# Kernel tuning notes

Hardware: AMD Instinct MI355X
Metric: run time of the kernel (lower is better)

## Reference

```python
import jax, jax.numpy as jnp
import numpy as np
from jax import lax

N_NEURONS = 128
BATCH = 2048
SEQ = 128
INFTY = 1e8


def setup_inputs() -> dict:
    key = jax.random.key(0)
    ks = jax.random.split(key, 10)
    n = N_NEURONS
    lim = 1.0 / np.sqrt(n)  # torch LSTMCell default init scale
    return {
        "enc_outputs": jax.random.normal(ks[0], (BATCH, SEQ, n), jnp.float32),
        "h0": jax.random.normal(ks[1], (BATCH, n), jnp.float32),
        "c0": jax.random.normal(ks[2], (BATCH, n), jnp.float32),
        "dec_first_input": jnp.zeros((1, n), jnp.float32),
        "W_ref": jax.random.normal(ks[3], (1, n, n), jnp.float32),
        "W_out": jax.random.normal(ks[4], (n, n), jnp.float32),
        "v": jax.random.normal(ks[5], (n,), jnp.float32),
        "W_ih": jax.random.uniform(ks[6], (4 * n, n), jnp.float32, -lim, lim),
        "W_hh": jax.random.uniform(ks[7], (4 * n, n), jnp.float32, -lim, lim),
        "b_ih": jax.random.uniform(ks[8], (4 * n,), jnp.float32, -lim, lim),
        "b_hh": jax.random.uniform(ks[9], (4 * n,), jnp.float32, -lim, lim),
    }


def _decode(enc_outputs, h0, c0, dec_first_input, W_ref, W_out, v, W_ih, W_hh, b_ih, b_hh):
    B, S, n = enc_outputs.shape
    # step-invariant pointer projection of encoder outputs (the conv1d term)
    enc_term = jnp.einsum("bsn,mn->bsm", enc_outputs, W_ref[0])  # [B,S,n]
    batch_idx = jnp.arange(B)
    keys = jax.random.split(jax.random.key(1234), S)
    inp0 = jnp.broadcast_to(dec_first_input, (B, n))
    mask0 = jnp.zeros((B, S), enc_outputs.dtype)

    def step(carry, key):
        h, c, mask, inp = carry
        # LSTMCell: gate order i, f, g, o (torch convention)
        gates = inp @ W_ih.T + b_ih + h @ W_hh.T + b_hh  # [B,4n]
        i_g, f_g, g_g, o_g = jnp.split(gates, 4, axis=1)
        c = jax.nn.sigmoid(f_g) * c + jax.nn.sigmoid(i_g) * jnp.tanh(g_g)
        h = jax.nn.sigmoid(o_g) * jnp.tanh(c)
        # pointer attention scores
        dec_term = (h @ W_out)[:, None, :]  # [B,1,n]
        scores = jnp.sum(v * jnp.tanh(enc_term + dec_term), axis=-1)  # [B,S]
        masked = scores - INFTY * mask
        loc = jax.random.categorical(key, masked)  # [B] int, non-differentiable sample
        logp = jnp.take_along_axis(jax.nn.log_softmax(masked, axis=1), loc[:, None], axis=1)[:, 0]
        mask = mask.at[batch_idx, loc].set(1.0)
        inp = enc_outputs[batch_idx, loc, :]  # gather next decoder input
        return (h, c, mask, inp), (loc, logp)

    _, (locs, logps) = lax.scan(step, (h0, c0, mask0, inp0), keys)
    locs = locs.T  # [B,S]
    tour = jnp.concatenate([locs, locs[:, :1]], axis=1)  # append first location
    log_prob = jnp.sum(logps, axis=0)  # [B]
    return log_prob, tour


def reference(enc_outputs, h0, c0, dec_first_input, W_ref, W_out, v, W_ih, W_hh, b_ih, b_hh):
    return _decode(enc_outputs, h0, c0, dec_first_input, W_ref, W_out, v, W_ih, W_hh, b_ih, b_hh)
```

## Files before the change

kernel.cpp:

```cpp
#include <hip/hip_runtime.h>
#include <cstdint>
#include <cstddef>

#pragma clang fp contract(off)

#define PRNG_PARTITIONABLE 1

#define INFTY_F 1.0e8f
#define TINY_F 1.17549435e-38f

__device__ __forceinline__ float fdiv_rn(float n, float q) {
  float y0 = __builtin_amdgcn_rcpf(q);
  float y  = fmaf(fmaf(-q, y0, 1.0f), y0, y0);
  float r0 = n * y;
  float e0 = fmaf(-q, r0, n);
  float r1 = fmaf(e0, y, r0);
  float e1 = fmaf(-q, r1, n);
  return fmaf(e1, y, r1);
}

__device__ __forceinline__ void tf2x32(uint32_t k0, uint32_t k1, uint32_t x0, uint32_t x1,
                                       uint32_t& o0, uint32_t& o1) {
  uint32_t ks2 = k0 ^ k1 ^ 0x1BD11BDAu;
  uint32_t v0 = x0 + k0, v1 = x1 + k1;
#define TF_R(r) { v0 += v1; v1 = (v1 << (r)) | (v1 >> (32 - (r))); v1 ^= v0; }
  TF_R(13) TF_R(15) TF_R(26) TF_R(6)
  v0 += k1;  v1 += ks2 + 1u;
  TF_R(17) TF_R(29) TF_R(16) TF_R(24)
  v0 += ks2; v1 += k0 + 2u;
  TF_R(13) TF_R(15) TF_R(26) TF_R(6)
  v0 += k0;  v1 += k1 + 3u;
  TF_R(17) TF_R(29) TF_R(16) TF_R(24)
  v0 += k1;  v1 += ks2 + 4u;
  TF_R(13) TF_R(15) TF_R(26) TF_R(6)
  v0 += ks2; v1 += k0 + 5u;
#undef TF_R
  o0 = v0; o1 = v1;
}

__device__ __forceinline__ uint32_t random_bits32(uint32_t k0, uint32_t k1, uint32_t j) {
#if PRNG_PARTITIONABLE
  uint32_t o0, o1;
  tf2x32(k0, k1, 0u, j, o0, o1);
  return o0 ^ o1;
#else
  uint32_t o0, o1;
  if (j < 131072u) { tf2x32(k0, k1, j, j + 131072u, o0, o1); return o0; }
  else             { tf2x32(k0, k1, j - 131072u, j, o0, o1); return o1; }
#endif
}

__device__ __forceinline__ float xla_tanhf(float x) {
  float xc = fminf(fmaxf(x, -9.0f), 9.0f);
  float x2 = xc * xc;
  float p = -2.76076847742355e-16f;
  p = (p * x2) + 2.00018790482477e-13f;
  p = (p * x2) + -8.60467152213735e-11f;
  p = (p * x2) + 5.12229709037114e-08f;
  p = (p * x2) + 1.48572235717979e-05f;
  p = (p * x2) + 6.37261928875436e-04f;
  p = (p * x2) + 4.89352455891786e-03f;
  float num = xc * p;
  float q = 1.19825839466702e-06f;
  q = (q * x2) + 1.18534705686654e-04f;
  q = (q * x2) + 2.26843463243900e-03f;
  q = (q * x2) + 4.89352518554385e-03f;
  float r = num / q;
  return (fabsf(x) < 0.0004f) ? x : r;
}

__device__ __forceinline__ void xla_tanh2(float xa, float xb, float& ra, float& rb) {
  float xca = fminf(fmaxf(xa, -9.0f), 9.0f);
  float xcb = fminf(fmaxf(xb, -9.0f), 9.0f);
  float x2a = xca * xca, x2b = xcb * xcb;
  float pa = -2.76076847742355e-16f, pb = -2.76076847742355e-16f;
  pa = (pa * x2a) + 2.00018790482477e-13f;  pb = (pb * x2b) + 2.00018790482477e-13f;
  pa = (pa * x2a) + -8.60467152213735e-11f; pb = (pb * x2b) + -8.60467152213735e-11f;
  pa = (pa * x2a) + 5.12229709037114e-08f;  pb = (pb * x2b) + 5.12229709037114e-08f;
  pa = (pa * x2a) + 1.48572235717979e-05f;  pb = (pb * x2b) + 1.48572235717979e-05f;
  pa = (pa * x2a) + 6.37261928875436e-04f;  pb = (pb * x2b) + 6.37261928875436e-04f;
  pa = (pa * x2a) + 4.89352455891786e-03f;  pb = (pb * x2b) + 4.89352455891786e-03f;
  float na = xca * pa, nb = xcb * pb;
  float qa = 1.19825839466702e-06f, qb = 1.19825839466702e-06f;
  qa = (qa * x2a) + 1.18534705686654e-04f; qb = (qb * x2b) + 1.18534705686654e-04f;
  qa = (qa * x2a) + 2.26843463243900e-03f; qb = (qb * x2b) + 2.26843463243900e-03f;
  qa = (qa * x2a) + 4.89352518554385e-03f; qb = (qb * x2b) + 4.89352518554385e-03f;
  float da = fdiv_rn(na, qa), db = fdiv_rn(nb, qb);
  ra = (fabsf(xa) < 0.0004f) ? xa : da;
  rb = (fabsf(xb) < 0.0004f) ? xb : db;
}

__device__ __forceinline__ float xla_expf(float x) {
  x = fminf(x, 88.3762626647950f);
  x = fmaxf(x, -88.3762626647949f);
  float m = floorf((x * 1.44269504088896341f) + 0.5f);
  float r = x - (m * 0.693359375f);
  r = r - (m * -2.12194440e-4f);
  float r2 = r * r;
  float y = 1.9875691500E-4f;
  y = (y * r) + 1.3981999507E-3f;
  y = (y * r) + 8.3334519073E-3f;
  y = (y * r) + 4.1665795894E-2f;
  y = (y * r) + 1.6666665459E-1f;
  y = (y * r) + 5.0000001201E-1f;
  y = (y * r2) + r;
  y = y + 1.0f;
  int mi = (int)m;
  float s = __uint_as_float((uint32_t)((mi + 127) << 23));
  return y * s;
}

__device__ __forceinline__ float xla_sigmoidf(float x) {
  return 1.0f / (1.0f + xla_expf(-x));
}

__device__ __forceinline__ float xla_logf(float x) {
  uint32_t b = __float_as_uint(x);
  float e = (float)((int)(b >> 23) - 126);
  float m = __uint_as_float((b & 0x007fffffu) | 0x3f000000u);
  bool mlt = (m < 0.707106781186547524f);
  float tmp = mlt ? m : 0.0f;
  e = e - (mlt ? 1.0f : 0.0f);
  float xx = (m - 1.0f) + tmp;
  float z = xx * xx;
  float y = 7.0376836292E-2f;
  y = (y * xx) + -1.1514610310E-1f;
  y = (y * xx) + 1.1676998740E-1f;
  y = (y * xx) + -1.2420140846E-1f;
  y = (y * xx) + 1.4249322787E-1f;
  y = (y * xx) + -1.6668057665E-1f;
  y = (y * xx) + 2.0000714765E-1f;
  y = (y * xx) + -2.4999993993E-1f;
  y = (y * xx) + 3.3333331174E-1f;
  y = y * xx;
  y = y * z;
  y = y + (e * -2.12194440e-4f);
  y = y - (z * 0.5f);
  float res = xx + y;
  res = res + (e * 0.693359375f);
  return res;
}

__device__ __forceinline__ float gumbel_from_bits(uint32_t bits) {
  float f = __uint_as_float((bits >> 9) | 0x3f800000u) - 1.0f;
  float u = (f * 1.0f) + TINY_F;
  u = fmaxf(TINY_F, u);
  return -xla_logf(-xla_logf(u));
}

__global__ void k_keys(uint32_t* __restrict__ keys) {
  int t = threadIdx.x;
  if (t >= 128) return;
#if PRNG_PARTITIONABLE
  uint32_t o0, o1;
  tf2x32(0u, 1234u, 0u, (uint32_t)t, o0, o1);
  keys[2 * t] = o0; keys[2 * t + 1] = o1;
#else
  uint32_t o0, o1, a, bb;
  if (t < 64) {
    tf2x32(0u, 1234u, (uint32_t)(2 * t),     (uint32_t)(128 + 2 * t), o0, o1); a  = o0;
    tf2x32(0u, 1234u, (uint32_t)(2 * t + 1), (uint32_t)(129 + 2 * t), o0, o1); bb = o0;
  } else {
    tf2x32(0u, 1234u, (uint32_t)(2 * t - 128), (uint32_t)(2 * t),     o0, o1); a  = o1;
    tf2x32(0u, 1234u, (uint32_t)(2 * t - 127), (uint32_t)(2 * t + 1), o0, o1); bb = o1;
  }
  keys[2 * t] = a; keys[2 * t + 1] = bb;
#endif
}

__global__ void k_trans(const float* __restrict__ Wih, const float* __restrict__ Whh,
                        float* __restrict__ WihT, float* __restrict__ WhhT) {
  int idx = blockIdx.x * blockDim.x + threadIdx.x;
  if (idx < 65536) {
    int r = idx >> 7, k = idx & 127;
    WihT[k * 512 + r] = Wih[idx];
    WhhT[k * 512 + r] = Whh[idx];
  }
}

__global__ __launch_bounds__(128) void k_encT(const float* __restrict__ enc,
                                              const float* __restrict__ Wref,
                                              float* __restrict__ encT) {
  __shared__ float el[64 * 132];
  __shared__ float ot[64 * 129];
  int tid = threadIdx.x;
  int b  = blockIdx.x >> 1;
  int sh = blockIdx.x & 1;
  const float* eb = enc + (size_t)b * 16384 + (size_t)sh * 8192;
  for (int i = tid; i < 8192; i += 128) {
    int s = i >> 7, n = i & 127;
    el[s * 132 + n] = eb[i];
  }
  __syncthreads();
  int sl = tid & 63;
  int mh = tid >> 6;
  for (int ml = 0; ml < 64; ++ml) {
    int m = mh * 64 + ml;
    const float4* wr = (const float4*)(Wref + m * 128);
    float acc = 0.0f;
#pragma unroll 8
    for (int q = 0; q < 32; ++q) {
      float4 w4 = wr[q];
      float4 e4 = *(const float4*)&el[sl * 132 + 4 * q];
      acc = fmaf(e4.x, w4.x, acc); acc = fmaf(e4.y, w4.y, acc);
      acc = fmaf(e4.z, w4.z, acc); acc = fmaf(e4.w, w4.w, acc);
    }
    ot[sl * 129 + m] = acc;
  }
  __syncthreads();
  float* op = encT + (size_t)b * 16384 + (size_t)(sh * 64) * 128;
  for (int i = tid; i < 8192; i += 128)
    op[i] = ot[(i >> 7) * 129 + (i & 127)];
}

__global__ __launch_bounds__(512) void k_encIH(const float* __restrict__ enc,
                                               const float* __restrict__ WihT,
                                               float* __restrict__ encIH) {
  __shared__ float el[32][128];
  const int r = threadIdx.x;
  const int b = blockIdx.x >> 2;
  const int q = blockIdx.x & 3;
  const float* eb = enc + (size_t)b * 16384 + (size_t)q * 4096;
  for (int i = r; i < 4096; i += 512)
    el[i >> 7][i & 127] = eb[i];
  __syncthreads();
  float acc[32];
#pragma unroll
  for (int s = 0; s < 32; ++s) acc[s] = 0.0f;
  const float* wp = WihT + r;
  for (int kc = 0; kc < 8; ++kc) {
    float wv[16];
#pragma unroll
    for (int j = 0; j < 16; ++j) wv[j] = wp[(size_t)(kc * 16 + j) * 512];
#pragma unroll
    for (int s = 0; s < 32; ++s) {
#pragma unroll
      for (int j = 0; j < 16; ++j)
        acc[s] = fmaf(el[s][kc * 16 + j], wv[j], acc[s]);
    }
  }
  float* op = encIH + ((size_t)b * 128 + (size_t)q * 32) * 512 + r;
#pragma unroll
  for (int s = 0; s < 32; ++s)
    op[(size_t)s * 512] = acc[s];
}

template <bool PRE>
__global__ __launch_bounds__(512, 4) void k_main(
    const float* __restrict__ enc, const float* __restrict__ h0,
    const float* __restrict__ c0, const float* __restrict__ dec_first,
    const float* __restrict__ W_out, const float* __restrict__ v,
    const float* __restrict__ b_ih, const float* __restrict__ b_hh,
    const float* __restrict__ WihT, const float* __restrict__ WhhT,
    const float* __restrict__ encT, const float* __restrict__ encIH,
    const uint32_t* __restrict__ keys, float* __restrict__ out) {
  __shared__ float xI_s[128][8];
  __shared__ float c_s[4][128];
  __shared__ float gates_s[4][512];
  __shared__ float2 vdec2_s[4][128];
  __shared__ float bih_s[512];
  __shared__ float bhh_s[512];
  __shared__ float v_s[128];
  __shared__ uint32_t keys_s[256];
  __shared__ int cu_s[4][128];
  __shared__ int pos_s[4][128];
  __shared__ int locs_s[4];
  __shared__ float red_va[4][2];
  __shared__ int   red_ia[4][2];
  __shared__ float red_mx[4][2];
  __shared__ float red_se[4][2];
  __shared__ float red_msel[4];

  const int tid  = threadIdx.x;
  const int lane = tid & 63;
  const int w    = tid >> 6;
  const int g4   = w >> 1;
  const int half = w & 1;
  const int s4   = half * 64 + lane;
  const int bbase = blockIdx.x * 4;
  const int b4   = bbase + g4;

  bih_s[tid] = b_ih[tid];
  bhh_s[tid] = b_hh[tid];
  if (tid < 256) keys_s[tid] = keys[tid];
  if (tid < 128) v_s[tid] = v[tid];
  {
    int g = tid >> 7, j = tid & 127;
    xI_s[j][g]     = dec_first[j];
    xI_s[j][4 + g] = h0[(size_t)(bbase + g) * 128 + j];
    c_s[g][j] = c0[(size_t)(bbase + g) * 128 + j];
    cu_s[g][j] = j;
    pos_s[g][j] = j;
  }
  float logp_sum = 0.0f;
  float* tour = out + 2048;
  __syncthreads();

  for (int step = 0; step < 128; ++step) {
    {
      const int r = tid;
      float aA0, aA1, aA2, aA3;
      float aB0 = 0.0f, aB1 = 0.0f, aB2 = 0.0f, aB3 = 0.0f;
      const float* phh = WhhT + r;
      if (PRE) {
        if (step == 0) {
          aA0 = aA1 = aA2 = aA3 = 0.0f;
        } else {
          aA0 = encIH[((size_t)(bbase + 0) * 128 + locs_s[0]) * 512 + r];
          aA1 = encIH[((size_t)(bbase + 1) * 128 + locs_s[1]) * 512 + r];
          aA2 = encIH[((size_t)(bbase + 2) * 128 + locs_s[2]) * 512 + r];
          aA3 = encIH[((size_t)(bbase + 3) * 128 + locs_s[3]) * 512 + r];
        }
#pragma unroll 4
        for (int k = 0; k < 128; ++k) {
          float4 xh = *(const float4*)&xI_s[k][4];
          float whh = phh[k * 512];
          aB0 = fmaf(xh.x, whh, aB0);
          aB1 = fmaf(xh.y, whh, aB1);
          aB2 = fmaf(xh.z, whh, aB2);
          aB3 = fmaf(xh.w, whh, aB3);
        }
      } else {
        aA0 = aA1 = aA2 = aA3 = 0.0f;
        const float* pih = WihT + r;
#pragma unroll 4
        for (int k = 0; k < 128; ++k) {
          float4 xi = *(const float4*)&xI_s[k][0];
          float4 xh = *(const float4*)&xI_s[k][4];
          float wih = pih[k * 512], whh = phh[k * 512];
          aA0 = fmaf(xi.x, wih, aA0);
          aA1 = fmaf(xi.y, wih, aA1);
          aA2 = fmaf(xi.z, wih, aA2);
          aA3 = fmaf(xi.w, wih, aA3);
          aB0 = fmaf(xh.x, whh, aB0);
          aB1 = fmaf(xh.y, whh, aB1);
          aB2 = fmaf(xh.z, whh, aB2);
          aB3 = fmaf(xh.w, whh, aB3);
        }
      }
      float b1 = bih_s[r], b2 = bhh_s[r];
      gates_s[0][r] = (((aA0 + b1) + aB0) + b2);
      gates_s[1][r] = (((aA1 + b1) + aB1) + b2);
      gates_s[2][r] = (((aA2 + b1) + aB2) + b2);
      gates_s[3][r] = (((aA3 + b1) + aB3) + b2);
    }
    __syncthreads();

    {
      int g = tid >> 7, j = tid & 127;
      float gi = gates_s[g][j], gf = gates_s[g][128 + j];
      float gg = gates_s[g][256 + j], go = gates_s[g][384 + j];
      float si = xla_sigmoidf(gi), sf = xla_sigmoidf(gf), so = xla_sigmoidf(go);
      float gt = xla_tanhf(gg);
      float cold = c_s[g][j];
      float cn = (sf * cold) + (si * gt);
      c_s[g][j] = cn;
      xI_s[j][4 + g] = so * xla_tanhf(cn);
    }
    __syncthreads();

    {
      int g = tid >> 7, m = tid & 127;
      float acc = 0.0f;
      const float* wo = W_out + m;
#pragma unroll 4
      for (int k = 0; k < 128; ++k)
        acc = fmaf(xI_s[k][4 + g], wo[k * 128], acc);
      vdec2_s[g][m] = make_float2(v_s[m], acc);
    }
    __syncthreads();

    const int u = 128 - step;
    const bool active = (s4 < u);
    float masked = -INFTY_F;
    float val = -INFTY_F;
    int   ia = 0x7fffffff;
    int   sc = 0;
    if (active) {
      sc = cu_s[g4][s4];
      const float* ep = encT + ((size_t)b4 * 128 + (size_t)sc) * 128;
      float acc = 0.0f;
#pragma unroll 4
      for (int m4 = 0; m4 < 32; ++m4) {
        float4 e4 = *(const float4*)&ep[4 * m4];
        float4 vd01 = *(const float4*)&vdec2_s[g4][4 * m4];
        float4 vd23 = *(const float4*)&vdec2_s[g4][4 * m4 + 2];
        float t0, t1, t2, t3;
        xla_tanh2(e4.x + vd01.y, e4.y + vd01.w, t0, t1);
        xla_tanh2(e4.z + vd23.y, e4.w + vd23.w, t2, t3);
        acc = acc + (vd01.x * t0);
        acc = acc + (vd01.z * t1);
        acc = acc + (vd23.x * t2);
        acc = acc + (vd23.z * t3);
      }
      masked = acc;
      uint32_t kk0 = keys_s[2 * step], kk1 = keys_s[2 * step + 1];
      uint32_t j0 = (uint32_t)b4 * 128u + (uint32_t)sc;
      float gmb = gumbel_from_bits(random_bits32(kk0, kk1, j0));
      val = gmb + masked;
      ia = sc;
    }
    {
      float va = val;
      float mx = masked;
#pragma unroll
      for (int off = 32; off > 0; off >>= 1) {
        float vo = __shfl_xor(va, off, 64);
        int io = __shfl_xor(ia, off, 64);
        if (vo > va || (vo == va && io < ia)) { va = vo; ia = io; }
        mx = fmaxf(mx, __shfl_xor(mx, off, 64));
      }
      float se = expf(masked - mx);
#pragma unroll
      for (int off = 32; off > 0; off >>= 1) se = se + __shfl_xor(se, off, 64);
      if (lane == 0) {
        red_va[g4][half] = va; red_ia[g4][half] = ia;
        red_mx[g4][half] = mx; red_se[g4][half] = se;
      }
      ia = active ? sc : 0x7fffffff;
    }
    __syncthreads();

    float mx2, lse2;
    {
      float vaA = red_va[g4][0], vaB = red_va[g4][1];
      int iaA = red_ia[g4][0], iaB = red_ia[g4][1];
      int loc = (vaB > vaA || (vaB == vaA && iaB < iaA)) ? iaB : iaA;
      if (active && sc == loc) {
        red_msel[g4] = masked;
        locs_s[g4] = loc;
        tour[(size_t)b4 * 129 + step] = (float)loc;
        if (step == 0) tour[(size_t)b4 * 129 + 128] = (float)loc;
        int p = pos_s[g4][loc];
        int last = cu_s[g4][u - 1];
        cu_s[g4][p] = last;
        pos_s[g4][last] = p;
      }
      const float* er = enc + (size_t)b4 * 16384 + (size_t)loc * 128;
      xI_s[s4][g4] = er[s4];
      float mxA = red_mx[g4][0], mxB = red_mx[g4][1];
      float seA = red_se[g4][0], seB = red_se[g4][1];
      mx2 = fmaxf(mxA, mxB);
      float se2 = seA * expf(mxA - mx2) + seB * expf(mxB - mx2);
      lse2 = logf(se2);
    }
    __syncthreads();
    logp_sum = logp_sum + ((red_msel[g4] - mx2) - lse2);
  }

  if (half == 0 && lane == 0) out[b4] = logp_sum;
}

extern "C" void kernel_launch(void* const* d_in, const int* in_sizes, int n_in,
                              void* d_out, int out_size, void* d_ws, size_t ws_size,
                              hipStream_t stream) {
  (void)in_sizes; (void)n_in; (void)out_size;
  const float* enc       = (const float*)d_in[0];
  const float* h0        = (const float*)d_in[1];
  const float* c0        = (const float*)d_in[2];
  const float* dec_first = (const float*)d_in[3];
  const float* W_ref     = (const float*)d_in[4];
  const float* W_out     = (const float*)d_in[5];
  const float* v         = (const float*)d_in[6];
  const float* W_ih      = (const float*)d_in[7];
  const float* W_hh      = (const float*)d_in[8];
  const float* b_ih      = (const float*)d_in[9];
  const float* b_hh      = (const float*)d_in[10];

  const size_t encT_elems  = (size_t)2048 * 16384;
  const size_t encIH_elems = (size_t)2048 * 128 * 512;
  size_t need_base = (encT_elems + 65536 + 65536) * sizeof(float) + 256 * sizeof(uint32_t);
  size_t need_pre  = need_base + encIH_elems * sizeof(float);
  if (ws_size < need_base) return;
  const bool pre = (ws_size >= need_pre);

  float* encT = (float*)d_ws;
  float* WihT = encT + encT_elems;
  float* WhhT = WihT + 65536;
  uint32_t* keys = (uint32_t*)(WhhT + 65536);
  float* encIH = (float*)(keys + 256);
  float* out = (float*)d_out;

  k_keys<<<dim3(1), dim3(128), 0, stream>>>(keys);
  k_trans<<<dim3(256), dim3(256), 0, stream>>>(W_ih, W_hh, WihT, WhhT);
  k_encT<<<dim3(4096), dim3(128), 0, stream>>>(enc, W_ref, encT);
  if (pre) {
    k_encIH<<<dim3(8192), dim3(512), 0, stream>>>(enc, WihT, encIH);
    k_main<true><<<dim3(512), dim3(512), 0, stream>>>(enc, h0, c0, dec_first, W_out, v,
                                                      b_ih, b_hh, WihT, WhhT, encT, encIH,
                                                      keys, out);
  } else {
    k_main<false><<<dim3(512), dim3(512), 0, stream>>>(enc, h0, c0, dec_first, W_out, v,
                                                       b_ih, b_hh, WihT, WhhT, encT, encIH,
                                                       keys, out);
  }
}
```

Baseline: 6.501 ms.

## Drop precomputed encoder-input gates and halve batch rows per block

Removes the k_encIH precompute pass and its large workspace buffer, so the input-to-hidden product is recomputed inside the step loop from WihT. Each block now handles 2 batch rows instead of 4 and the grid doubles to 1024 blocks, with launch bounds raised to 8 blocks per CU. The aim is more parallelism across the GPU and no large precompute write/read. The cost is that each step redoes the Wih matvec, and half the waves sit idle in the pointer phase while still joining the barriers.

```diff
diff --git a/kernel.cpp b/kernel.cpp
--- a/kernel.cpp
+++ b/kernel.cpp
@@ -213,81 +213,48 @@
     op[i] = ot[(i >> 7) * 129 + (i & 127)];
 }
 
-__global__ __launch_bounds__(512) void k_encIH(const float* __restrict__ enc,
-                                               const float* __restrict__ WihT,
-                                               float* __restrict__ encIH) {
-  __shared__ float el[32][128];
-  const int r = threadIdx.x;
-  const int b = blockIdx.x >> 2;
-  const int q = blockIdx.x & 3;
-  const float* eb = enc + (size_t)b * 16384 + (size_t)q * 4096;
-  for (int i = r; i < 4096; i += 512)
-    el[i >> 7][i & 127] = eb[i];
-  __syncthreads();
-  float acc[32];
-#pragma unroll
-  for (int s = 0; s < 32; ++s) acc[s] = 0.0f;
-  const float* wp = WihT + r;
-  for (int kc = 0; kc < 8; ++kc) {
-    float wv[16];
-#pragma unroll
-    for (int j = 0; j < 16; ++j) wv[j] = wp[(size_t)(kc * 16 + j) * 512];
-#pragma unroll
-    for (int s = 0; s < 32; ++s) {
-#pragma unroll
-      for (int j = 0; j < 16; ++j)
-        acc[s] = fmaf(el[s][kc * 16 + j], wv[j], acc[s]);
-    }
-  }
-  float* op = encIH + ((size_t)b * 128 + (size_t)q * 32) * 512 + r;
-#pragma unroll
-  for (int s = 0; s < 32; ++s)
-    op[(size_t)s * 512] = acc[s];
-}
-
-template <bool PRE>
-__global__ __launch_bounds__(512, 4) void k_main(
+__global__ __launch_bounds__(512, 8) void k_main(
     const float* __restrict__ enc, const float* __restrict__ h0,
     const float* __restrict__ c0, const float* __restrict__ dec_first,
     const float* __restrict__ W_out, const float* __restrict__ v,
     const float* __restrict__ b_ih, const float* __restrict__ b_hh,
     const float* __restrict__ WihT, const float* __restrict__ WhhT,
-    const float* __restrict__ encT, const float* __restrict__ encIH,
-    const uint32_t* __restrict__ keys, float* __restrict__ out) {
-  __shared__ float xI_s[128][8];
-  __shared__ float c_s[4][128];
-  __shared__ float gates_s[4][512];
-  __shared__ float2 vdec2_s[4][128];
+    const float* __restrict__ encT, const uint32_t* __restrict__ keys,
+    float* __restrict__ out) {
+  __shared__ float xI_s[128][4];
+  __shared__ float c_s[2][128];
+  __shared__ float gates_s[2][512];
+  __shared__ float2 vdec2_s[2][128];
   __shared__ float bih_s[512];
   __shared__ float bhh_s[512];
   __shared__ float v_s[128];
   __shared__ uint32_t keys_s[256];
-  __shared__ int cu_s[4][128];
-  __shared__ int pos_s[4][128];
-  __shared__ int locs_s[4];
-  __shared__ float red_va[4][2];
-  __shared__ int   red_ia[4][2];
-  __shared__ float red_mx[4][2];
-  __shared__ float red_se[4][2];
-  __shared__ float red_msel[4];
+  __shared__ int cu_s[2][128];
+  __shared__ int pos_s[2][128];
+  __shared__ float red_va[2][2];
+  __shared__ int   red_ia[2][2];
+  __shared__ float red_mx[2][2];
+  __shared__ float red_se[2][2];
+  __shared__ float red_msel[2];
 
   const int tid  = threadIdx.x;
   const int lane = tid & 63;
   const int w    = tid >> 6;
+  const bool pwave = (w < 4);
   const int g4   = w >> 1;
   const int half = w & 1;
   const int s4   = half * 64 + lane;
-  const int bbase = blockIdx.x * 4;
-  const int b4   = bbase + g4;
+  const int bbase = blockIdx.x * 2;
+  const int b4   = bbase + (pwave ? g4 : 0);
 
   bih_s[tid] = b_ih[tid];
   bhh_s[tid] = b_hh[tid];
   if (tid < 256) keys_s[tid] = keys[tid];
-  if (tid < 128) v_s[tid] = v[tid];
-  {
+  if (tid >= 256 && tid < 384) v_s[tid - 256] = v[tid - 256];
+  if (tid < 256) {
     int g = tid >> 7, j = tid & 127;
     xI_s[j][g]     = dec_first[j];
-    xI_s[j][4 + g] = h0[(size_t)(bbase + g) * 128 + j];
+    xI_s[j][2 + g] = h0[(size_t)(bbase + g) * 128 + j];
     c_s[g][j] = c0[(size_t)(bbase + g) * 128 + j];
     cu_s[g][j] = j;
     pos_s[g][j] = j;
@@ -299,54 +266,26 @@
   for (int step = 0; step < 128; ++step) {
     {
       const int r = tid;
-      float aA0, aA1, aA2, aA3;
-      float aB0 = 0.0f, aB1 = 0.0f, aB2 = 0.0f, aB3 = 0.0f;
+      float aA0 = 0.0f, aA1 = 0.0f, aB0 = 0.0f, aB1 = 0.0f;
+      const float* pih = WihT + r;
       const float* phh = WhhT + r;
-      if (PRE) {
-        if (step == 0) {
-          aA0 = aA1 = aA2 = aA3 = 0.0f;
-        } else {
-          aA0 = encIH[((size_t)(bbase + 0) * 128 + locs_s[0]) * 512 + r];
-          aA1 = encIH[((size_t)(bbase + 1) * 128 + locs_s[1]) * 512 + r];
-          aA2 = encIH[((size_t)(bbase + 2) * 128 + locs_s[2]) * 512 + r];
-          aA3 = encIH[((size_t)(bbase + 3) * 128 + locs_s[3]) * 512 + r];
-        }
 #pragma unroll 4
-        for (int k = 0; k < 128; ++k) {
-          float4 xh = *(const float4*)&xI_s[k][4];
-          float whh = phh[k * 512];
-          aB0 = fmaf(xh.x, whh, aB0);
-          aB1 = fmaf(xh.y, whh, aB1);
-          aB2 = fmaf(xh.z, whh, aB2);
-          aB3 = fmaf(xh.w, whh, aB3);
-        }
-      } else {
-        aA0 = aA1 = aA2 = aA3 = 0.0f;
-        const float* pih = WihT + r;
-#pragma unroll 4
-        for (int k = 0; k < 128; ++k) {
-          float4 xi = *(const float4*)&xI_s[k][0];
-          float4 xh = *(const float4*)&xI_s[k][4];
-          float wih = pih[k * 512], whh = phh[k * 512];
-          aA0 = fmaf(xi.x, wih, aA0);
-          aA1 = fmaf(xi.y, wih, aA1);
-          aA2 = fmaf(xi.z, wih, aA2);
-          aA3 = fmaf(xi.w, wih, aA3);
-          aB0 = fmaf(xh.x, whh, aB0);
-          aB1 = fmaf(xh.y, whh, aB1);
-          aB2 = fmaf(xh.z, whh, aB2);
-          aB3 = fmaf(xh.w, whh, aB3);
-        }
+      for (int k = 0; k < 128; ++k) {
+        float2 xi = *(const float2*)&xI_s[k][0];
+        float2 xh = *(const float2*)&xI_s[k][2];
+        float wih = pih[k * 512], whh = phh[k * 512];
+        aA0 = fmaf(xi.x, wih, aA0);
+        aA1 = fmaf(xi.y, wih, aA1);
+        aB0 = fmaf(xh.x, whh, aB0);
+        aB1 = fmaf(xh.y, whh, aB1);
       }
       float b1 = bih_s[r], b2 = bhh_s[r];
       gates_s[0][r] = (((aA0 + b1) + aB0) + b2);
       gates_s[1][r] = (((aA1 + b1) + aB1) + b2);
-      gates_s[2][r] = (((aA2 + b1) + aB2) + b2);
-      gates_s[3][r] = (((aA3 + b1) + aB3) + b2);
     }
     __syncthreads();
 
-    {
+    if (tid < 256) {
       int g = tid >> 7, j = tid & 127;
       float gi = gates_s[g][j], gf = gates_s[g][128 + j];
       float gg = gates_s[g][256 + j], go = gates_s[g][384 + j];
@@ -355,52 +294,52 @@
       float cold = c_s[g][j];
       float cn = (sf * cold) + (si * gt);
       c_s[g][j] = cn;
-      xI_s[j][4 + g] = so * xla_tanhf(cn);
+      xI_s[j][2 + g] = so * xla_tanhf(cn);
     }
     __syncthreads();
 
-    {
+    if (tid < 256) {
       int g = tid >> 7, m = tid & 127;
       float acc = 0.0f;
       const float* wo = W_out + m;
 #pragma unroll 4
       for (int k = 0; k < 128; ++k)
-        acc = fmaf(xI_s[k][4 + g], wo[k * 128], acc);
+        acc = fmaf(xI_s[k][2 + g], wo[k * 128], acc);
       vdec2_s[g][m] = make_float2(v_s[m], acc);
     }
     __syncthreads();
 
     const int u = 128 - step;
-    const bool active = (s4 < u);
-    float masked = -INFTY_F;
-    float val = -INFTY_F;
-    int   ia = 0x7fffffff;
-    int   sc = 0;
-    if (active) {
-      sc = cu_s[g4][s4];
-      const float* ep = encT + ((size_t)b4 * 128 + (size_t)sc) * 128;
-      float acc = 0.0f;
+    if (pwave) {
+      const bool active = (s4 < u);
+      float masked = -INFTY_F;
+      float val = -INFTY_F;
+      int   ia = 0x7fffffff;
+      int   sc = 0;
+      if (active) {
+        sc = cu_s[g4][s4];
+        const float* ep = encT + ((size_t)b4 * 128 + (size_t)sc) * 128;
+        float acc = 0.0f;
 #pragma unroll 4
-      for (int m4 = 0; m4 < 32; ++m4) {
-        float4 e4 = *(const float4*)&ep[4 * m4];
-        float4 vd01 = *(const float4*)&vdec2_s[g4][4 * m4];
-        float4 vd23 = *(const float4*)&vdec2_s[g4][4 * m4 + 2];
-        float t0, t1, t2, t3;
-        xla_tanh2(e4.x + vd01.y, e4.y + vd01.w, t0, t1);
-        xla_tanh2(e4.z + vd23.y, e4.w + vd23.w, t2, t3);
-        acc = acc + (vd01.x * t0);
-        acc = acc + (vd01.z * t1);
-        acc = acc + (vd23.x * t2);
-        acc = acc + (vd23.z * t3);
+        for (int m4 = 0; m4 < 32; ++m4) {
+          float4 e4 = *(const float4*)&ep[4 * m4];
+          float4 vd01 = *(const float4*)&vdec2_s[g4][4 * m4];
+          float4 vd23 = *(const float4*)&vdec2_s[g4][4 * m4 + 2];
+          float t0, t1, t2, t3;
+          xla_tanh2(e4.x + vd01.y, e4.y + vd01.w, t0, t1);
+          xla_tanh2(e4.z + vd23.y, e4.w + vd23.w, t2, t3);
+          acc = acc + (vd01.x * t0);
+          acc = acc + (vd01.z * t1);
+          acc = acc + (vd23.x * t2);
+          acc = acc + (vd23.z * t3);
+        }
+        masked = acc;
+        uint32_t kk0 = keys_s[2 * step], kk1 = keys_s[2 * step + 1];
+        uint32_t j0 = (uint32_t)b4 * 128u + (uint32_t)sc;
+        float gmb = gumbel_from_bits(random_bits32(kk0, kk1, j0));
+        val = gmb + masked;
+        ia = sc;
       }
-      masked = acc;
-      uint32_t kk0 = keys_s[2 * step], kk1 = keys_s[2 * step + 1];
-      uint32_t j0 = (uint32_t)b4 * 128u + (uint32_t)sc;
-      float gmb = gumbel_from_bits(random_bits32(kk0, kk1, j0));
-      val = gmb + masked;
-      ia = sc;
-    }
-    {
       float va = val;
       float mx = masked;
 #pragma unroll
@@ -417,38 +356,38 @@
         red_va[g4][half] = va; red_ia[g4][half] = ia;
         red_mx[g4][half] = mx; red_se[g4][half] = se;
       }
-      ia = active ? sc : 0x7fffffff;
+      __syncthreads();
+
+      {
+        float vaA = red_va[g4][0], vaB = red_va[g4][1];
+        int iaA = red_ia[g4][0], iaB = red_ia[g4][1];
+        int loc = (vaB > vaA || (vaB == vaA && iaB < iaA)) ? iaB : iaA;
+        if (active && sc == loc) {
+          red_msel[g4] = masked;
+          tour[(size_t)b4 * 129 + step] = (float)loc;
+          if (step == 0) tour[(size_t)b4 * 129 + 128] = (float)loc;
+          int p = pos_s[g4][loc];
+          int last = cu_s[g4][u - 1];
+          cu_s[g4][p] = last;
+          pos_s[g4][last] = p;
+        }
+        const float* er = enc + (size_t)b4 * 16384 + (size_t)loc * 128;
+        xI_s[s4][g4] = er[s4];
+        float mxA = red_mx[g4][0], mxB = red_mx[g4][1];
+        float seA = red_se[g4][0], seB = red_se[g4][1];
+        float mx2 = fmaxf(mxA, mxB);
+        float se2 = seA * expf(mxA - mx2) + seB * expf(mxB - mx2);
+        float lse2 = logf(se2);
+        __syncthreads();
+        logp_sum = logp_sum + ((red_msel[g4] - mx2) - lse2);
+      }
+    } else {
+      __syncthreads();
+      __syncthreads();
     }
-    __syncthreads();
-
-    float mx2, lse2;
-    {
-      float vaA = red_va[g4][0], vaB = red_va[g4][1];
-      int iaA = red_ia[g4][0], iaB = red_ia[g4][1];
-      int loc = (vaB > vaA || (vaB == vaA && iaB < iaA)) ? iaB : iaA;
-      if (active && sc == loc) {
-        red_msel[g4] = masked;
-        locs_s[g4] = loc;
-        tour[(size_t)b4 * 129 + step] = (float)loc;
-        if (step == 0) tour[(size_t)b4 * 129 + 128] = (float)loc;
-        int p = pos_s[g4][loc];
-        int last = cu_s[g4][u - 1];
-        cu_s[g4][p] = last;
-        pos_s[g4][last] = p;
-      }
-      const float* er = enc + (size_t)b4 * 16384 + (size_t)loc * 128;
-      xI_s[s4][g4] = er[s4];
-      float mxA = red_mx[g4][0], mxB = red_mx[g4][1];
-      float seA = red_se[g4][0], seB = red_se[g4][1];
-      mx2 = fmaxf(mxA, mxB);
-      float se2 = seA * expf(mxA - mx2) + seB * expf(mxB - mx2);
-      lse2 = logf(se2);
-    }
-    __syncthreads();
-    logp_sum = logp_sum + ((red_msel[g4] - mx2) - lse2);
-  }
-
-  if (half == 0 && lane == 0) out[b4] = logp_sum;
+  }
+
+  if (pwave && half == 0 && lane == 0) out[b4] = logp_sum;
 }
 
 extern "C" void kernel_launch(void* const* d_in, const int* in_sizes, int n_in,
@@ -467,31 +406,19 @@
   const float* b_ih      = (const float*)d_in[9];
   const float* b_hh      = (const float*)d_in[10];
 
-  const size_t encT_elems  = (size_t)2048 * 16384;
-  const size_t encIH_elems = (size_t)2048 * 128 * 512;
-  size_t need_base = (encT_elems + 65536 + 65536) * sizeof(float) + 256 * sizeof(uint32_t);
-  size_t need_pre  = need_base + encIH_elems * sizeof(float);
-  if (ws_size < need_base) return;
-  const bool pre = (ws_size >= need_pre);
+  const size_t encT_elems = (size_t)2048 * 16384;
+  size_t need = (encT_elems + 65536 + 65536) * sizeof(float) + 256 * sizeof(uint32_t);
+  if (ws_size < need) return;
 
   float* encT = (float*)d_ws;
   float* WihT = encT + encT_elems;
   float* WhhT = WihT + 65536;
   uint32_t* keys = (uint32_t*)(WhhT + 65536);
-  float* encIH = (float*)(keys + 256);
   float* out = (float*)d_out;
 
   k_keys<<<dim3(1), dim3(128), 0, stream>>>(keys);
   k_trans<<<dim3(256), dim3(256), 0, stream>>>(W_ih, W_hh, WihT, WhhT);
   k_encT<<<dim3(4096), dim3(128), 0, stream>>>(enc, W_ref, encT);
-  if (pre) {
-    k_encIH<<<dim3(8192), dim3(512), 0, stream>>>(enc, WihT, encIH);
-    k_main<true><<<dim3(512), dim3(512), 0, stream>>>(enc, h0, c0, dec_first, W_out, v,
-                                                      b_ih, b_hh, WihT, WhhT, encT, encIH,
-                                                      keys, out);
-  } else {
-    k_main<false><<<dim3(512), dim3(512), 0, stream>>>(enc, h0, c0, dec_first, W_out, v,
-                                                       b_ih, b_hh, WihT, WhhT, encT, encIH,
-                                                       keys, out);
-  }
-}
+  k_main<<<dim3(1024), dim3(512), 0, stream>>>(enc, h0, c0, dec_first, W_out, v,
+                                               b_ih, b_hh, WihT, WhhT, encT, keys, out);
+}
```

After: 7.682 ms. 1.18x slower.
